# Kernel optimization log

Measured on AMD Instinct MI355X. Metric: run time of the kernel, lower is better.

## Reference

```python
import jax, jax.numpy as jnp
import numpy as np

SS, D, V = 64, 256, 10000
B, S = 16, 512


def setup_inputs() -> dict:
    key = jax.random.key(0)
    ks = jax.random.split(key, 7)
    scale = lambda fan_in: 1.0 / np.sqrt(fan_in)
    return {
        "x": jax.random.normal(ks[0], (B, S, D), dtype=jnp.float32),
        # nn.Linear(D, 4*ss): weight [4ss, D], bias [4ss]
        "Wxs_w": jax.random.uniform(ks[1], (4 * SS, D), jnp.float32, -scale(D), scale(D)),
        "Wxs_b": jax.random.uniform(ks[2], (4 * SS,), jnp.float32, -scale(D), scale(D)),
        # nn.Linear(ss, 4*ss)
        "Wss_w": jax.random.uniform(ks[3], (4 * SS, SS), jnp.float32, -scale(SS), scale(SS)),
        "Wss_b": jax.random.uniform(ks[4], (4 * SS,), jnp.float32, -scale(SS), scale(SS)),
        # nn.Linear(ss, V)
        "Wsy_w": jax.random.uniform(ks[5], (V, SS), jnp.float32, -scale(SS), scale(SS)),
        "Wsy_b": jax.random.uniform(ks[6], (V,), jnp.float32, -scale(SS), scale(SS)),
    }


def reference(x, Wxs_w, Wxs_b, Wss_w, Wss_b, Wsy_w, Wsy_b):
    b, s, _ = x.shape
    ss = Wss_w.shape[1]
    # Precompute input projections for all timesteps: [s, b, 4ss]
    xproj = jnp.einsum("bsd,kd->sbk", x, Wxs_w) + Wxs_b

    def step(carry, xp_t):
        h, c = carry
        comb = xp_t + h @ Wss_w.T + Wss_b  # [b, 4ss]
        f, i, g, o = jnp.split(comb, 4, axis=-1)
        f = jax.nn.sigmoid(f)
        i = jax.nn.sigmoid(i)
        o = jax.nn.sigmoid(o)
        g = jnp.tanh(g)
        c = c * f + i * g
        h = o * c  # NOTE: original code omits tanh(c) here; stay faithful
        return (h, c), h

    h0 = jnp.zeros((b, ss), dtype=x.dtype)
    c0 = jnp.zeros((b, ss), dtype=x.dtype)
    _, hs = jax.lax.scan(step, (h0, c0), xproj)  # hs: [s, b, ss]
    # Per-step vocab projection == batched projection of stacked hidden states
    y = jnp.einsum("sbh,vh->bsv", hs, Wsy_w) + Wsy_b  # [b, s, V]
    return y
```

## Files before the change

kernel.cpp:

```cpp
#include <hip/hip_runtime.h>

typedef unsigned short u16;
typedef unsigned int u32;

using short8 = __attribute__((ext_vector_type(8))) short;
using f32x4  = __attribute__((ext_vector_type(4))) float;
using f32x2  = __attribute__((ext_vector_type(2))) float;

#define SSEQ 512
#define BB   16
#define DD   256
#define G4   256
#define SSZ  64
#define VV   10000
#define VPAD 10112
#define MALL 8192

#define OFF_XHI   0u
#define OFF_XLO   4194304u
#define OFF_WHI   8388608u
#define OFF_WLO   8519680u
#define OFF_WSY   8650752u
#define OFF_XPROJ 9945088u
#define OFF_HS    18333696u

__device__ __forceinline__ u16 f2bf(float f) {
  u32 u = __float_as_uint(f);
  u32 r = (u + 0x7fffu + ((u >> 16) & 1u)) >> 16;
  return (u16)r;
}
__device__ __forceinline__ float bf2f(u16 h) {
  return __uint_as_float(((u32)h) << 16);
}
__device__ __forceinline__ float sigm(float x) {
  float e = exp2f(-1.442695041f * x);
  return __builtin_amdgcn_rcpf(1.f + e);
}
__device__ __forceinline__ float tanh_fast(float x) {
  float xc = fminf(fmaxf(x, -20.f), 20.f);
  float z = exp2f(2.885390082f * xc);
  return (z - 1.f) * __builtin_amdgcn_rcpf(z + 1.f);
}
__device__ __forceinline__ f32x2 pkfma(f32x2 a, f32x2 b, f32x2 c) {
  asm("v_pk_fma_f32 %0, %1, %2, %0" : "+v"(c) : "v"(a), "v"(b));
  return c;
}

#define NX 2097152
#define NW 65536
#define NP 647168
__global__ void k0_convert(const float* __restrict__ x, const float* __restrict__ Wxs,
                           const float* __restrict__ Wsy,
                           u16* __restrict__ xhi, u16* __restrict__ xlo,
                           u16* __restrict__ whi, u16* __restrict__ wlo,
                           u16* __restrict__ wsyb) {
  int i = blockIdx.x * 256 + threadIdx.x;
  if (i < NX) {
    float v = x[i]; u16 h = f2bf(v);
    xhi[i] = h; xlo[i] = f2bf(v - bf2f(h));
  } else if (i < NX + NW) {
    int j = i - NX;
    float v = Wxs[j]; u16 h = f2bf(v);
    whi[j] = h; wlo[j] = f2bf(v - bf2f(h));
  } else if (i < NX + NW + NP) {
    int j = i - NX - NW;
    wsyb[j] = (j < VV * SSZ) ? f2bf(Wsy[j]) : (u16)0;
  }
}

__global__ __launch_bounds__(256) void k1_xproj(
    const u16* __restrict__ xhi, const u16* __restrict__ xlo,
    const u16* __restrict__ whi, const u16* __restrict__ wlo,
    const float* __restrict__ bias, float* __restrict__ xproj) {
  int bid = blockIdx.x;
  int mb = bid >> 1, nb = bid & 1;
  int tid = threadIdx.x, l = tid & 63, wid = tid >> 6;
  int wm = wid >> 1, wv = wid & 1;
  int m0 = mb * 128 + wm * 64, n0 = nb * 128 + wv * 64;
  int lr = l & 15, lg = l >> 4;

  f32x4 acc[4][4];
#pragma unroll
  for (int a = 0; a < 4; a++)
#pragma unroll
    for (int bq = 0; bq < 4; bq++) acc[a][bq] = (f32x4){0.f, 0.f, 0.f, 0.f};

#pragma unroll
  for (int p = 0; p < 3; p++) {
    const u16* A = (p == 1) ? xlo : xhi;
    const u16* B = (p == 2) ? wlo : whi;
#pragma unroll
    for (int ks = 0; ks < 8; ks++) {
      short8 af[4], bf_[4];
#pragma unroll
      for (int fm = 0; fm < 4; fm++)
        af[fm] = *(const short8*)(A + (size_t)(m0 + fm * 16 + lr) * 256 + ks * 32 + lg * 8);
#pragma unroll
      for (int fv = 0; fv < 4; fv++)
        bf_[fv] = *(const short8*)(B + (size_t)(n0 + fv * 16 + lr) * 256 + ks * 32 + lg * 8);
#pragma unroll
      for (int fm = 0; fm < 4; fm++)
#pragma unroll
        for (int fv = 0; fv < 4; fv++)
          acc[fm][fv] = __builtin_amdgcn_mfma_f32_16x16x32_bf16(af[fm], bf_[fv], acc[fm][fv], 0, 0, 0);
    }
  }
#pragma unroll
  for (int fv = 0; fv < 4; fv++) {
    int j = n0 + fv * 16 + lr;
    float bj = bias[j];
#pragma unroll
    for (int fm = 0; fm < 4; fm++)
#pragma unroll
      for (int r = 0; r < 4; r++) {
        int m = m0 + fm * 16 + lg * 4 + r;
        xproj[(size_t)m * 256 + j] = acc[fm][fv][r] + bj;
      }
  }
}

__global__ __launch_bounds__(256, 1) void k2_scan(
    const float* __restrict__ xproj, const float* __restrict__ Wss,
    const float* __restrict__ Wssb, u16* __restrict__ hsb) {
  __shared__ float gact[4][64];
  __shared__ float hbuf[64];
  __shared__ u16 hstage[SSEQ][64];

  int b = blockIdx.x, tid = threadIdx.x;
  int w = tid >> 6, j = tid & 63;

  f32x2 wr[32];
  const f32x2* pw = (const f32x2*)(Wss + (size_t)(w * 64 + j) * 64);
#pragma unroll
  for (int q = 0; q < 32; q++) wr[q] = pw[q];
  float bg = Wssb[w * 64 + j];

  f32x4 h4[16];
#pragma unroll
  for (int q = 0; q < 16; q++) h4[q] = (f32x4){0.f, 0.f, 0.f, 0.f};
  float c = 0.f;

  const float* xpb = xproj + (size_t)b * SSEQ * 256 + w * 64 + j;
  float xp0 = xpb[0];
  float xp1 = xpb[256];

  for (int t = 0; t < SSEQ; t++) {
    float xp2 = (t + 2 < SSEQ) ? xpb[(size_t)(t + 2) * 256] : 0.f;

    f32x2 a0 = (f32x2){bg + xp0, 0.f};
    f32x2 a1 = (f32x2){0.f, 0.f};
    f32x2 a2 = (f32x2){0.f, 0.f};
    f32x2 a3 = (f32x2){0.f, 0.f};
#pragma unroll
    for (int q = 0; q < 8; q++) {
      f32x2 hA0 = (f32x2){h4[2 * q][0], h4[2 * q][1]};
      f32x2 hB0 = (f32x2){h4[2 * q][2], h4[2 * q][3]};
      f32x2 hA1 = (f32x2){h4[2 * q + 1][0], h4[2 * q + 1][1]};
      f32x2 hB1 = (f32x2){h4[2 * q + 1][2], h4[2 * q + 1][3]};
      a0 = pkfma(hA0, wr[4 * q + 0], a0);
      a1 = pkfma(hB0, wr[4 * q + 1], a1);
      a2 = pkfma(hA1, wr[4 * q + 2], a2);
      a3 = pkfma(hB1, wr[4 * q + 3], a3);
    }
    float a = (a0[0] + a0[1]) + (a1[0] + a1[1]) + ((a2[0] + a2[1]) + (a3[0] + a3[1]));

    float act = (w == 2) ? tanh_fast(a) : sigm(a);
    gact[w][j] = act;
    asm volatile("s_waitcnt lgkmcnt(0)\n\ts_barrier" ::: "memory");

    float fg = gact[0][j], ig = gact[1][j], gg = gact[2][j], og = gact[3][j];
    c = fmaf(c, fg, ig * gg);
    float hn = og * c;

    if (w == 0) {
      hbuf[j] = hn;
      hstage[t][j] = f2bf(hn);
    }
    asm volatile("s_waitcnt lgkmcnt(0)\n\ts_barrier" ::: "memory");

    const f32x4* hb = (const f32x4*)hbuf;
#pragma unroll
    for (int q = 0; q < 16; q++) h4[q] = hb[q];

    xp0 = xp1; xp1 = xp2;
  }

  __syncthreads();
  const uint4* src = (const uint4*)hstage;
  uint4* dst = (uint4*)(hsb + (size_t)b * SSEQ * 64);
#pragma unroll
  for (int i = 0; i < 16; i++) dst[tid + 256 * i] = src[tid + 256 * i];
}

__global__ __launch_bounds__(256) void k3_y(
    const u16* __restrict__ hsb, const u16* __restrict__ wsyb,
    const float* __restrict__ bias, float* __restrict__ y) {
  int bid = blockIdx.x;
  int mb = bid / 79, vb = bid - mb * 79;
  int tid = threadIdx.x, l = tid & 63, wid = tid >> 6;
  int wm = wid >> 1, wv = wid & 1;
  int m0 = mb * 128 + wm * 64, v0 = vb * 128 + wv * 64;
  int lr = l & 15, lg = l >> 4;

  f32x4 acc[4][4];
#pragma unroll
  for (int a = 0; a < 4; a++)
#pragma unroll
    for (int bq = 0; bq < 4; bq++) acc[a][bq] = (f32x4){0.f, 0.f, 0.f, 0.f};

#pragma unroll
  for (int ks = 0; ks < 2; ks++) {
    short8 af[4], bf_[4];
#pragma unroll
    for (int fm = 0; fm < 4; fm++)
      af[fm] = *(const short8*)(hsb + (size_t)(m0 + fm * 16 + lr) * 64 + ks * 32 + lg * 8);
#pragma unroll
    for (int fv = 0; fv < 4; fv++)
      bf_[fv] = *(const short8*)(wsyb + (size_t)(v0 + fv * 16 + lr) * 64 + ks * 32 + lg * 8);
#pragma unroll
    for (int fv = 0; fv < 4; fv++)
#pragma unroll
      for (int fm = 0; fm < 4; fm++)
        acc[fv][fm] = __builtin_amdgcn_mfma_f32_16x16x32_bf16(bf_[fv], af[fm], acc[fv][fm], 0, 0, 0);
  }

#pragma unroll
  for (int fv = 0; fv < 4; fv++) {
    int vb4 = v0 + fv * 16 + lg * 4;
    bool ok = (vb4 + 3) < VV;
    float4 bv = ok ? *(const float4*)(bias + vb4) : float4{0.f, 0.f, 0.f, 0.f};
#pragma unroll
    for (int fm = 0; fm < 4; fm++) {
      int m = m0 + fm * 16 + lr;
      if (ok) {
        float4 o;
        o.x = acc[fv][fm][0] + bv.x;
        o.y = acc[fv][fm][1] + bv.y;
        o.z = acc[fv][fm][2] + bv.z;
        o.w = acc[fv][fm][3] + bv.w;
        *(float4*)(y + (size_t)m * (size_t)VV + vb4) = o;
      }
    }
  }
}

extern "C" void kernel_launch(void* const* d_in, const int* in_sizes, int n_in,
                              void* d_out, int out_size, void* d_ws, size_t ws_size,
                              hipStream_t stream) {
  const float* x     = (const float*)d_in[0];
  const float* Wxs_w = (const float*)d_in[1];
  const float* Wxs_b = (const float*)d_in[2];
  const float* Wss_w = (const float*)d_in[3];
  const float* Wss_b = (const float*)d_in[4];
  const float* Wsy_w = (const float*)d_in[5];
  const float* Wsy_b = (const float*)d_in[6];
  float* y = (float*)d_out;
  char* ws = (char*)d_ws;

  u16*   xhi   = (u16*)(ws + OFF_XHI);
  u16*   xlo   = (u16*)(ws + OFF_XLO);
  u16*   whi   = (u16*)(ws + OFF_WHI);
  u16*   wlo   = (u16*)(ws + OFF_WLO);
  u16*   wsyb  = (u16*)(ws + OFF_WSY);
  float* xproj = (float*)(ws + OFF_XPROJ);
  u16*   hsb   = (u16*)(ws + OFF_HS);

  k0_convert<<<(NX + NW + NP) / 256, 256, 0, stream>>>(x, Wxs_w, Wsy_w, xhi, xlo, whi, wlo, wsyb);
  k1_xproj<<<128, 256, 0, stream>>>(xhi, xlo, whi, wlo, Wxs_b, xproj);
  k2_scan<<<16, 256, 0, stream>>>(xproj, Wss_w, Wss_b, hsb);
  k3_y<<<64 * 79, 256, 0, stream>>>(hsb, wsyb, Wsy_b, y);
}
```

Baseline: 331.8 us.

## Remap scan gates into each wave and exchange via shuffles, dropping one barrier

The recurrent scan kernel used to give each wave one whole gate type, so gate activations had to go through shared memory with an extra block barrier every step. Now each wave holds all four gates for 16 hidden units and exchanges them with cross-lane shuffles. Only the barrier for publishing h remains, and h is double-buffered so one barrier per step is enough. Sigmoid and tanh are merged into one branch-free exp/rcp formula with per-lane constants, which may slightly change tanh accuracy because the clamp is removed.

```diff
diff --git a/kernel.cpp b/kernel.cpp
--- a/kernel.cpp
+++ b/kernel.cpp
@@ -31,15 +31,6 @@
 }
 __device__ __forceinline__ float bf2f(u16 h) {
   return __uint_as_float(((u32)h) << 16);
-}
-__device__ __forceinline__ float sigm(float x) {
-  float e = exp2f(-1.442695041f * x);
-  return __builtin_amdgcn_rcpf(1.f + e);
-}
-__device__ __forceinline__ float tanh_fast(float x) {
-  float xc = fminf(fmaxf(x, -20.f), 20.f);
-  float z = exp2f(2.885390082f * xc);
-  return (z - 1.f) * __builtin_amdgcn_rcpf(z + 1.f);
 }
 __device__ __forceinline__ f32x2 pkfma(f32x2 a, f32x2 b, f32x2 c) {
   asm("v_pk_fma_f32 %0, %1, %2, %0" : "+v"(c) : "v"(a), "v"(b));
@@ -122,25 +113,31 @@
 __global__ __launch_bounds__(256, 1) void k2_scan(
     const float* __restrict__ xproj, const float* __restrict__ Wss,
     const float* __restrict__ Wssb, u16* __restrict__ hsb) {
-  __shared__ float gact[4][64];
-  __shared__ float hbuf[64];
+  __shared__ float hbuf[2][64];
   __shared__ u16 hstage[SSEQ][64];
 
   int b = blockIdx.x, tid = threadIdx.x;
-  int w = tid >> 6, j = tid & 63;
+  int w = tid >> 6, l = tid & 63;
+  int s = l & 15, g = l >> 4;
+  int jj = w * 16 + s;
+  int row = g * 64 + jj;
 
   f32x2 wr[32];
-  const f32x2* pw = (const f32x2*)(Wss + (size_t)(w * 64 + j) * 64);
+  const f32x2* pw = (const f32x2*)(Wss + (size_t)row * 64);
 #pragma unroll
   for (int q = 0; q < 32; q++) wr[q] = pw[q];
-  float bg = Wssb[w * 64 + j];
+  float bg = Wssb[row];
+
+  float kk = (g == 2) ? 2.885390082f : -1.442695041f;
+  float Ac = (g == 2) ? 1.f : 0.f;
+  float Bc = (g == 2) ? -2.f : 1.f;
 
   f32x4 h4[16];
 #pragma unroll
   for (int q = 0; q < 16; q++) h4[q] = (f32x4){0.f, 0.f, 0.f, 0.f};
   float c = 0.f;
 
-  const float* xpb = xproj + (size_t)b * SSEQ * 256 + w * 64 + j;
+  const float* xpb = xproj + (size_t)b * SSEQ * 256 + row;
   float xp0 = xpb[0];
   float xp1 = xpb[256];
 
@@ -162,23 +159,26 @@
       a2 = pkfma(hA1, wr[4 * q + 2], a2);
       a3 = pkfma(hB1, wr[4 * q + 3], a3);
     }
-    float a = (a0[0] + a0[1]) + (a1[0] + a1[1]) + ((a2[0] + a2[1]) + (a3[0] + a3[1]));
-
-    float act = (w == 2) ? tanh_fast(a) : sigm(a);
-    gact[w][j] = act;
-    asm volatile("s_waitcnt lgkmcnt(0)\n\ts_barrier" ::: "memory");
-
-    float fg = gact[0][j], ig = gact[1][j], gg = gact[2][j], og = gact[3][j];
+    float a = ((a0[0] + a0[1]) + (a1[0] + a1[1])) + ((a2[0] + a2[1]) + (a3[0] + a3[1]));
+
+    float z = exp2f(kk * a);
+    float act = fmaf(Bc, __builtin_amdgcn_rcpf(z + 1.f), Ac);
+
+    float fg = __shfl(act, s, 64);
+    float ig = __shfl(act, 16 + s, 64);
+    float gg = __shfl(act, 32 + s, 64);
+    float og = __shfl(act, 48 + s, 64);
+
     c = fmaf(c, fg, ig * gg);
     float hn = og * c;
 
-    if (w == 0) {
-      hbuf[j] = hn;
-      hstage[t][j] = f2bf(hn);
+    if (g == 0) {
+      hbuf[t & 1][jj] = hn;
+      hstage[t][jj] = f2bf(hn);
     }
     asm volatile("s_waitcnt lgkmcnt(0)\n\ts_barrier" ::: "memory");
 
-    const f32x4* hb = (const f32x4*)hbuf;
+    const f32x4* hb = (const f32x4*)hbuf[t & 1];
 #pragma unroll
     for (int q = 0; q < 16; q++) h4[q] = hb[q];
 
```

After: 328.4 us. Within noise of the previous version (-1.0%).
